# Performance work log

Hardware: AMD Instinct MI355X
Metric: run time of the kernel (lower is better)

## Reference

```python
import jax, jax.numpy as jnp
import numpy as np

N, M = 100000, 12
A, E = 128, 64
BN_EPS = 1e-5

def batchnorm(x, gamma, beta):
    # training-mode BN over leading dim, biased variance (torch default)
    mean = jnp.mean(x, axis=0)
    var = jnp.var(x, axis=0)
    return (x - mean) * jax.lax.rsqrt(var + BN_EPS) * gamma + beta

def setup_inputs() -> dict:
    key = jax.random.key(0)
    ks = jax.random.split(key, 9)
    s_in = 1.0 / np.sqrt(2 * A + E)
    s_skip = 1.0 / np.sqrt(A)
    return {
        "atom_in_fea": jax.random.normal(ks[0], (N, A), jnp.float32),
        "nbr_fea": jax.random.normal(ks[1], (N, M, E), jnp.float32),
        "nbr_fea_idx": jax.random.randint(ks[2], (N, M), 0, N),
        "W_full": jax.random.uniform(ks[3], (2 * A + E, 2 * A), jnp.float32, -s_in, s_in),
        "b_full": jax.random.uniform(ks[4], (2 * A,), jnp.float32, -s_in, s_in),
        "gamma1": jnp.ones((2 * A,), jnp.float32),
        "beta1": jnp.zeros((2 * A,), jnp.float32),
        "gamma2": jnp.ones((A,), jnp.float32),
        "beta2": jnp.zeros((A,), jnp.float32),
        "W_skip": jax.random.uniform(ks[5], (A, A), jnp.float32, -s_skip, s_skip),
        "b_skip": jax.random.uniform(ks[6], (A,), jnp.float32, -s_skip, s_skip),
    }

def reference(atom_in_fea, nbr_fea, nbr_fea_idx, W_full, b_full,
              gamma1, beta1, gamma2, beta2, W_skip, b_skip):
    atom_nbr_fea = atom_in_fea[nbr_fea_idx]                      # [N,M,A] gather
    atom_self_fea = jnp.broadcast_to(atom_in_fea[:, None, :], (N, M, A))
    total = jnp.concatenate([atom_self_fea, atom_nbr_fea, nbr_fea], axis=2)  # [N,M,2A+E]
    gated = jnp.einsum('nmf,fg->nmg', total, W_full) + b_full    # [N,M,2A]
    gated = batchnorm(gated.reshape(-1, 2 * A), gamma1, beta1).reshape(N, M, 2 * A)
    nbr_filter, nbr_core = gated[..., :A], gated[..., A:]
    nbr_sumed = jnp.sum(jax.nn.sigmoid(nbr_filter) * jax.nn.softplus(nbr_core), axis=1)  # [N,A]
    nbr_sumed = batchnorm(nbr_sumed, gamma2, beta2)
    skip_val = atom_in_fea @ W_skip + b_skip
    return jax.nn.softplus(skip_val + nbr_sumed)
```

## Files before the change

### kernel.cpp

```cpp
#include <hip/hip_runtime.h>
#include <stdint.h>

#define N_ATOM 100000
#define M_NBR 12
#define A_FEA 128
#define E_FEA 64
#define KDIM 320
#define GDIM 256
#define ROWS (N_ATOM*M_NBR)
#define BN_EPS 1e-5f

typedef unsigned short u16;
typedef unsigned int u32;
typedef __attribute__((ext_vector_type(8))) short short8;
typedef __attribute__((ext_vector_type(4))) float f32x4;

#define S_BN1SUM 0
#define S_BN1SSQ 256
#define S_S1 512
#define S_T1 768
#define S_BN2SUM 1024
#define S_BN2SSQ 1152
#define S_S2 1280
#define S_T2 1408
#define STATS_F32 1536

#define WPQ_OFF 0
#define W3_OFF 131072
#define WSK_OFF 163840
#define STATS_OFF 196608
#define P_OFF 202752
#define PQ_BYTES ((size_t)N_ATOM*256*2)
#define Q_OFF (P_OFF + PQ_BYTES)
#define NEED_MID (Q_OFF + PQ_BYTES)

__device__ __forceinline__ u16 f2bf(float x) {
    union { float f; u32 u; } v; v.f = x;
    u32 r = v.u + 0x7FFFu + ((v.u >> 16) & 1u);
    return (u16)(r >> 16);
}
__device__ __forceinline__ float bf2f(u16 u) {
    union { u32 u; float f; } v; v.u = ((u32)u) << 16;
    return v.f;
}
__device__ __forceinline__ float softplus_f(float x) {
    return fmaxf(x, 0.f) + __logf(1.f + __expf(-fabsf(x)));
}
__device__ __forceinline__ float sigmoid_f(float x) {
    return 1.f / (1.f + __expf(-x));
}

__global__ void zero_stats(float* __restrict__ stats) {
    int t = threadIdx.x;
    stats[t] = 0.f;
    stats[256 + t] = 0.f;
    stats[1024 + t] = 0.f;
}

__global__ void finalize1(const float* __restrict__ g1, const float* __restrict__ b1,
                          float* __restrict__ stats) {
    int c = threadIdx.x;
    const float inv_cnt = 1.f / (float)ROWS;
    float mean = stats[S_BN1SUM + c] * inv_cnt;
    float var  = stats[S_BN1SSQ + c] * inv_cnt - mean * mean;
    float iv = rsqrtf(var + BN_EPS);
    float s = g1[c] * iv;
    stats[S_S1 + c] = s;
    stats[S_T1 + c] = fmaf(-mean, s, b1[c]);
}

__global__ void finalize2(const float* __restrict__ g2, const float* __restrict__ b2,
                          float* __restrict__ stats) {
    int c = threadIdx.x;
    const float inv_cnt = 1.f / (float)N_ATOM;
    float mean = stats[S_BN2SUM + c] * inv_cnt;
    float var  = stats[S_BN2SSQ + c] * inv_cnt - mean * mean;
    float iv = rsqrtf(var + BN_EPS);
    float s = g2[c] * iv;
    stats[S_S2 + c] = s;
    stats[S_T2 + c] = fmaf(-mean, s, b2[c]);
}

__global__ void prep_pack_fast(const float* __restrict__ Wfull,
                               const float* __restrict__ Wskip,
                               u16* __restrict__ wpq, u16* __restrict__ w3,
                               u16* __restrict__ wsk) {
    int tid = blockIdx.x * blockDim.x + threadIdx.x;
    int l = tid & 63, fr = l & 15, fq = l >> 4;
    if (tid < 8192) {
        int ct = (tid >> 6) & 31;
        int kt = tid >> 11;
        int c = ct * 16 + fr;
        int k0 = kt * 32 + fq * 8;
        u16 tmp[8];
        #pragma unroll
        for (int i = 0; i < 8; ++i) {
            int kk = k0 + i;
            float v = (c < 256) ? Wfull[kk * GDIM + c]
                                : Wfull[(128 + kk) * GDIM + (c - 256)];
            tmp[i] = f2bf(v);
        }
        uint4 pk;
        pk.x = (u32)tmp[0] | ((u32)tmp[1] << 16);
        pk.y = (u32)tmp[2] | ((u32)tmp[3] << 16);
        pk.z = (u32)tmp[4] | ((u32)tmp[5] << 16);
        pk.w = (u32)tmp[6] | ((u32)tmp[7] << 16);
        *reinterpret_cast<uint4*>(&wpq[tid * 8]) = pk;
    } else if (tid < 10240) {
        int t2 = tid - 8192;
        int ct = (t2 >> 6) & 15;
        int kt = t2 >> 10;
        int c = ct * 16 + fr;
        int k0 = kt * 32 + fq * 8;
        u16 tmp[8];
        #pragma unroll
        for (int i = 0; i < 8; ++i) tmp[i] = f2bf(Wfull[(256 + k0 + i) * GDIM + c]);
        uint4 pk;
        pk.x = (u32)tmp[0] | ((u32)tmp[1] << 16);
        pk.y = (u32)tmp[2] | ((u32)tmp[3] << 16);
        pk.z = (u32)tmp[4] | ((u32)tmp[5] << 16);
        pk.w = (u32)tmp[6] | ((u32)tmp[7] << 16);
        *reinterpret_cast<uint4*>(&w3[t2 * 8]) = pk;
    } else if (tid < 12288) {
        int t3 = tid - 10240;
        int ct = (t3 >> 6) & 7;
        int kt = t3 >> 9;
        int c = ct * 16 + fr;
        int k0 = kt * 32 + fq * 8;
        u16 tmp[8];
        #pragma unroll
        for (int i = 0; i < 8; ++i) tmp[i] = f2bf(Wskip[(k0 + i) * A_FEA + c]);
        uint4 pk;
        pk.x = (u32)tmp[0] | ((u32)tmp[1] << 16);
        pk.y = (u32)tmp[2] | ((u32)tmp[3] << 16);
        pk.z = (u32)tmp[4] | ((u32)tmp[5] << 16);
        pk.w = (u32)tmp[6] | ((u32)tmp[7] << 16);
        *reinterpret_cast<uint4*>(&wsk[t3 * 8]) = pk;
    }
}

__launch_bounds__(256)
__global__ void pq_kernel(const float* __restrict__ atom_in,
                          const u16* __restrict__ wpq,
                          u16* __restrict__ Pb, u16* __restrict__ Qb) {
    __shared__ u16 al[64 * 130];
    const int t = threadIdx.x;
    const int w = t >> 6, l = t & 63, fr = l & 15, fq = l >> 4;
    const int n0 = blockIdx.x * 64;

    #pragma unroll
    for (int it = 0; it < 4; ++it) {
        int c = t + it * 256;
        int row = c >> 4, seg = c & 15;
        int n = n0 + row;
        uint4 pk = {0u, 0u, 0u, 0u};
        if (n < N_ATOM) {
            const float* src = atom_in + (size_t)n * A_FEA + seg * 8;
            float4 x0 = *reinterpret_cast<const float4*>(src);
            float4 x1 = *reinterpret_cast<const float4*>(src + 4);
            pk.x = (u32)f2bf(x0.x) | ((u32)f2bf(x0.y) << 16);
            pk.y = (u32)f2bf(x0.z) | ((u32)f2bf(x0.w) << 16);
            pk.z = (u32)f2bf(x1.x) | ((u32)f2bf(x1.y) << 16);
            pk.w = (u32)f2bf(x1.z) | ((u32)f2bf(x1.w) << 16);
        }
        *reinterpret_cast<uint4*>(&al[row * 130 + seg * 8]) = pk;
    }
    __syncthreads();

    f32x4 acc[4][8];
    #pragma unroll
    for (int rt = 0; rt < 4; ++rt)
        #pragma unroll
        for (int p = 0; p < 8; ++p)
            acc[rt][p] = (f32x4){0.f,0.f,0.f,0.f};

    for (int kt = 0; kt < 4; ++kt) {
        short8 af[4], bf[8];
        #pragma unroll
        for (int rt = 0; rt < 4; ++rt)
            af[rt] = *reinterpret_cast<const short8*>(
                &al[(rt * 16 + fr) * 130 + kt * 32 + fq * 8]);
        #pragma unroll
        for (int p = 0; p < 8; ++p)
            bf[p] = *reinterpret_cast<const short8*>(
                &wpq[((kt * 32 + w * 8 + p) * 64 + l) * 8]);
        #pragma unroll
        for (int rt = 0; rt < 4; ++rt)
            #pragma unroll
            for (int p = 0; p < 8; ++p)
                acc[rt][p] = __builtin_amdgcn_mfma_f32_16x16x32_bf16(
                    af[rt], bf[p], acc[rt][p], 0, 0, 0);
    }

    #pragma unroll
    for (int p = 0; p < 8; ++p) {
        int col = w * 128 + p * 16 + fr;
        u16* dst = (col < 256) ? Pb : Qb;
        int cc = (col < 256) ? col : (col - 256);
        #pragma unroll
        for (int rt = 0; rt < 4; ++rt)
            #pragma unroll
            for (int j = 0; j < 4; ++j) {
                int n = n0 + rt * 16 + fq * 4 + j;
                if (n < N_ATOM) dst[(size_t)n * 256 + cc] = f2bf(acc[rt][p][j]);
            }
    }
}

#define NTILES_E (ROWS/96)
#define GRID_E 2500
#define EPAD 66
#define PPAD 264
#define QPAD 268
#define ACTPAD2 134
#define P_SH (96*EPAD*2)
#define Q_SH (P_SH + 8*PPAD*2)
#define SH_TOTAL (Q_SH + 96*QPAD*2)

template<int MODE>
__launch_bounds__(512, 4)
__global__ void estage2(const float* __restrict__ nbr_fea,
                        const int* __restrict__ nbr_idx,
                        const u16* __restrict__ w3,
                        const u16* __restrict__ Pb,
                        const u16* __restrict__ Qb,
                        float* __restrict__ stats,
                        float* __restrict__ out_ns) {
    __shared__ __align__(16) unsigned char shraw[SH_TOTAL];
    u16* e_lds = (u16*)shraw;
    u16* p_lds = (u16*)(shraw + P_SH);
    u16* q_lds = (u16*)(shraw + Q_SH);
    float* act = (float*)(shraw + Q_SH);
    float* red = (float*)shraw;

    const int t = threadIdx.x;
    const int w = t >> 6, l = t & 63, fr = l & 15, fq = l >> 4;
    const int col0 = w * 16 + fr;
    const int col1 = 128 + col0;

    float s1v0 = 0.f, t1v0 = 0.f, s1v1 = 0.f, t1v1 = 0.f;
    if (MODE == 2) {
        s1v0 = stats[S_S1 + col0]; t1v0 = stats[S_T1 + col0];
        s1v1 = stats[S_S1 + col1]; t1v1 = stats[S_T1 + col1];
    }
    float ls0 = 0.f, lq0 = 0.f, ls1 = 0.f, lq1 = 0.f;
    float bsum = 0.f, bssq = 0.f;

    for (int tile = blockIdx.x; tile < NTILES_E; tile += GRID_E) {
        const int r0 = tile * 96;
        const int n0a = tile * 8;

        __syncthreads();

        #pragma unroll
        for (int i = 0; i < 2; ++i) {
            int o = t + i * 512;
            if (o < 768) {
                int row = o >> 3, seg = o & 7;
                const float* src = nbr_fea + (size_t)(r0 + row) * E_FEA + seg * 8;
                float4 x0 = *reinterpret_cast<const float4*>(src);
                float4 x1 = *reinterpret_cast<const float4*>(src + 4);
                uint4 pk;
                pk.x = (u32)f2bf(x0.x) | ((u32)f2bf(x0.y) << 16);
                pk.y = (u32)f2bf(x0.z) | ((u32)f2bf(x0.w) << 16);
                pk.z = (u32)f2bf(x1.x) | ((u32)f2bf(x1.y) << 16);
                pk.w = (u32)f2bf(x1.z) | ((u32)f2bf(x1.w) << 16);
                *reinterpret_cast<uint4*>(&e_lds[row * EPAD + seg * 8]) = pk;
            }
        }
        if (t < 256) {
            int row = t >> 5, seg = t & 31;
            *reinterpret_cast<uint4*>(&p_lds[row * PPAD + seg * 8]) =
                *reinterpret_cast<const uint4*>(&Pb[(size_t)(n0a + row) * 256 + seg * 8]);
        }
        #pragma unroll
        for (int i = 0; i < 12; ++i) {
            int row = i * 8 + w;
            int jr = nbr_idx[r0 + row];
            *reinterpret_cast<uint2*>(&q_lds[row * QPAD + l * 4]) =
                *reinterpret_cast<const uint2*>(&Qb[(size_t)jr * 256 + l * 4]);
        }
        __syncthreads();

        f32x4 acc[6][2];
        #pragma unroll
        for (int rt = 0; rt < 6; ++rt) {
            acc[rt][0] = (f32x4){0.f,0.f,0.f,0.f};
            acc[rt][1] = (f32x4){0.f,0.f,0.f,0.f};
        }
        #pragma unroll
        for (int kt = 0; kt < 2; ++kt) {
            short8 af[6], bf0, bf1;
            #pragma unroll
            for (int rt = 0; rt < 6; ++rt)
                af[rt] = *reinterpret_cast<const short8*>(
                    &e_lds[(rt * 16 + fr) * EPAD + kt * 32 + fq * 8]);
            bf0 = *reinterpret_cast<const short8*>(&w3[((kt * 16 + w) * 64 + l) * 8]);
            bf1 = *reinterpret_cast<const short8*>(&w3[((kt * 16 + 8 + w) * 64 + l) * 8]);
            #pragma unroll
            for (int rt = 0; rt < 6; ++rt) {
                acc[rt][0] = __builtin_amdgcn_mfma_f32_16x16x32_bf16(af[rt], bf0, acc[rt][0], 0, 0, 0);
                acc[rt][1] = __builtin_amdgcn_mfma_f32_16x16x32_bf16(af[rt], bf1, acc[rt][1], 0, 0, 0);
            }
        }

        if (MODE == 1) {
            #pragma unroll
            for (int rt = 0; rt < 6; ++rt)
                #pragma unroll
                for (int j = 0; j < 4; ++j) {
                    int row = rt * 16 + fq * 4 + j;
                    int atom = (row * 171) >> 11;
                    float g0 = acc[rt][0][j] + bf2f(p_lds[atom * PPAD + col0])
                                             + bf2f(q_lds[row * QPAD + col0]);
                    float g1 = acc[rt][1][j] + bf2f(p_lds[atom * PPAD + col1])
                                             + bf2f(q_lds[row * QPAD + col1]);
                    ls0 += g0; lq0 = fmaf(g0, g0, lq0);
                    ls1 += g1; lq1 = fmaf(g1, g1, lq1);
                }
        } else {
            float ar[24];
            #pragma unroll
            for (int rt = 0; rt < 6; ++rt)
                #pragma unroll
                for (int j = 0; j < 4; ++j) {
                    int row = rt * 16 + fq * 4 + j;
                    int atom = (row * 171) >> 11;
                    float g0 = acc[rt][0][j] + bf2f(p_lds[atom * PPAD + col0])
                                             + bf2f(q_lds[row * QPAD + col0]);
                    float g1 = acc[rt][1][j] + bf2f(p_lds[atom * PPAD + col1])
                                             + bf2f(q_lds[row * QPAD + col1]);
                    float gf = fmaf(g0, s1v0, t1v0);
                    float gc = fmaf(g1, s1v1, t1v1);
                    ar[rt * 4 + j] = sigmoid_f(gf) * softplus_f(gc);
                }
            __syncthreads();
            #pragma unroll
            for (int rt = 0; rt < 6; ++rt)
                #pragma unroll
                for (int j = 0; j < 4; ++j) {
                    int row = rt * 16 + fq * 4 + j;
                    act[row * ACTPAD2 + col0] = ar[rt * 4 + j];
                }
            __syncthreads();
            #pragma unroll
            for (int i = 0; i < 2; ++i) {
                int o = i * 512 + t;
                int a = o >> 7;
                int c = t & 127;
                float S = 0.f;
                #pragma unroll
                for (int mm = 0; mm < 12; ++mm)
                    S += act[(a * 12 + mm) * ACTPAD2 + c];
                out_ns[(size_t)(n0a + a) * A_FEA + c] = S;
                bsum += S;
                bssq = fmaf(S, S, bssq);
            }
        }
    }

    if (MODE == 1) {
        float s, q;
        s = ls0 + __shfl_xor(ls0, 16, 64); s += __shfl_xor(s, 32, 64);
        q = lq0 + __shfl_xor(lq0, 16, 64); q += __shfl_xor(q, 32, 64);
        if (fq == 0) {
            atomicAdd(&stats[S_BN1SUM + col0], s);
            atomicAdd(&stats[S_BN1SSQ + col0], q);
        }
        s = ls1 + __shfl_xor(ls1, 16, 64); s += __shfl_xor(s, 32, 64);
        q = lq1 + __shfl_xor(lq1, 16, 64); q += __shfl_xor(q, 32, 64);
        if (fq == 0) {
            atomicAdd(&stats[S_BN1SUM + col1], s);
            atomicAdd(&stats[S_BN1SSQ + col1], q);
        }
    } else {
        __syncthreads();
        if (t >= 128) {
            red[(t - 128) * 2]     = bsum;
            red[(t - 128) * 2 + 1] = bssq;
        }
        __syncthreads();
        if (t < 128) {
            bsum += red[t * 2]     + red[(128 + t) * 2]     + red[(256 + t) * 2];
            bssq += red[t * 2 + 1] + red[(128 + t) * 2 + 1] + red[(256 + t) * 2 + 1];
            atomicAdd(&stats[S_BN2SUM + t], bsum);
            atomicAdd(&stats[S_BN2SSQ + t], bssq);
        }
    }
}

#define BM5 64
__launch_bounds__(256, 2)
__global__ void skip_kernel(const float* __restrict__ atom_in,
                            const u16* __restrict__ wsf,
                            const float* __restrict__ b_skip,
                            const float* __restrict__ stats,
                            float* __restrict__ out) {
    __shared__ u16 a5[BM5 * 136];
    const int t = threadIdx.x;
    const int w = t >> 6, l = t & 63, fr = l & 15, fq = l >> 4;
    const int n0 = blockIdx.x * BM5;

    #pragma unroll
    for (int it = 0; it < 4; ++it) {
        int c = t + it * 256;
        int row = c >> 4, seg = c & 15;
        int n = n0 + row;
        uint4 pk = {0u, 0u, 0u, 0u};
        if (n < N_ATOM) {
            const float* src = atom_in + (size_t)n * A_FEA + seg * 8;
            float4 x0 = *reinterpret_cast<const float4*>(src);
            float4 x1 = *reinterpret_cast<const float4*>(src + 4);
            pk.x = (u32)f2bf(x0.x) | ((u32)f2bf(x0.y) << 16);
            pk.y = (u32)f2bf(x0.z) | ((u32)f2bf(x0.w) << 16);
            pk.z = (u32)f2bf(x1.x) | ((u32)f2bf(x1.y) << 16);
            pk.w = (u32)f2bf(x1.z) | ((u32)f2bf(x1.w) << 16);
        }
        *reinterpret_cast<uint4*>(&a5[row * 136 + seg * 8]) = pk;
    }
    __syncthreads();

    f32x4 acc[4][2];
    #pragma unroll
    for (int rt = 0; rt < 4; ++rt) {
        acc[rt][0] = (f32x4){0.f,0.f,0.f,0.f};
        acc[rt][1] = (f32x4){0.f,0.f,0.f,0.f};
    }
    for (int kt = 0; kt < 4; ++kt) {
        short8 af[4], bf[2];
        #pragma unroll
        for (int rt = 0; rt < 4; ++rt)
            af[rt] = *reinterpret_cast<const short8*>(
                &a5[(rt * 16 + fr) * 136 + kt * 32 + fq * 8]);
        #pragma unroll
        for (int p = 0; p < 2; ++p)
            bf[p] = *reinterpret_cast<const short8*>(
                &wsf[((kt * 8 + 2 * w + p) * 64 + l) * 8]);
        #pragma unroll
        for (int rt = 0; rt < 4; ++rt)
            #pragma unroll
            for (int p = 0; p < 2; ++p)
                acc[rt][p] = __builtin_amdgcn_mfma_f32_16x16x32_bf16(
                    af[rt], bf[p], acc[rt][p], 0, 0, 0);
    }

    #pragma unroll
    for (int p = 0; p < 2; ++p) {
        int col = w * 32 + p * 16 + fr;
        float bs = b_skip[col];
        float s2 = stats[S_S2 + col];
        float t2 = stats[S_T2 + col];
        #pragma unroll
        for (int rt = 0; rt < 4; ++rt)
            #pragma unroll
            for (int j = 0; j < 4; ++j) {
                int n = n0 + rt * 16 + fq * 4 + j;
                if (n < N_ATOM) {
                    size_t o = (size_t)n * A_FEA + col;
                    float S = out[o];
                    out[o] = softplus_f(acc[rt][p][j] + bs + fmaf(S, s2, t2));
                }
            }
    }
}

#define BM 96
#define NTILES (ROWS/BM)
#define GRID_P 2500
#define TPB 256
#define APAD 328
#define ACTPAD 132

__global__ void prep_pack_slow(const float* __restrict__ Wfull,
                               const float* __restrict__ Wskip,
                               u16* __restrict__ wf, u16* __restrict__ wsf) {
    int tid = blockIdx.x * blockDim.x + threadIdx.x;
    if (tid < 10240) {
        int l = tid & 63;
        int ct = (tid >> 6) & 15;
        int kt = tid >> 10;
        int fr = l & 15, fq = l >> 4;
        int col = ct * 16 + fr;
        int k0 = kt * 32 + fq * 8;
        u16 tmp[8];
        #pragma unroll
        for (int i = 0; i < 8; ++i) tmp[i] = f2bf(Wfull[(k0 + i) * GDIM + col]);
        uint4 pk;
        pk.x = (u32)tmp[0] | ((u32)tmp[1] << 16);
        pk.y = (u32)tmp[2] | ((u32)tmp[3] << 16);
        pk.z = (u32)tmp[4] | ((u32)tmp[5] << 16);
        pk.w = (u32)tmp[6] | ((u32)tmp[7] << 16);
        *reinterpret_cast<uint4*>(&wf[tid * 8]) = pk;
    } else if (tid < 12288) {
        int t2 = tid - 10240;
        int l = t2 & 63;
        int ct = (t2 >> 6) & 7;
        int kt = t2 >> 9;
        int fr = l & 15, fq = l >> 4;
        int col = ct * 16 + fr;
        int k0 = kt * 32 + fq * 8;
        u16 tmp[8];
        #pragma unroll
        for (int i = 0; i < 8; ++i) tmp[i] = f2bf(Wskip[(k0 + i) * A_FEA + col]);
        uint4 pk;
        pk.x = (u32)tmp[0] | ((u32)tmp[1] << 16);
        pk.y = (u32)tmp[2] | ((u32)tmp[3] << 16);
        pk.z = (u32)tmp[4] | ((u32)tmp[5] << 16);
        pk.w = (u32)tmp[6] | ((u32)tmp[7] << 16);
        *reinterpret_cast<uint4*>(&wsf[t2 * 8]) = pk;
    }
}

template<int PASS>
__launch_bounds__(TPB, 2)
__global__ void pass_kernel(const float* __restrict__ atom_in,
                            const float* __restrict__ nbr_fea,
                            const int* __restrict__ nbr_idx,
                            const u16* __restrict__ wf,
                            float* __restrict__ stats,
                            float* __restrict__ out_ns) {
    __shared__ union {
        u16 a[BM * APAD];
        float act[BM * ACTPAD];
    } sh;

    const int t = threadIdx.x;
    const int w = t >> 6, l = t & 63, fr = l & 15, fq = l >> 4;
    const int ct0 = 2 * w;

    int colp[4];
    colp[0] = ct0 * 16 + fr;
    colp[1] = colp[0] + 16;
    colp[2] = colp[0] + 128;
    colp[3] = colp[1] + 128;

    float s1v[4], t1v[4];
    if (PASS == 2) {
        #pragma unroll
        for (int p = 0; p < 4; ++p) {
            s1v[p] = stats[S_S1 + colp[p]];
            t1v[p] = stats[S_T1 + colp[p]];
        }
    }
    float ls[4] = {0.f,0.f,0.f,0.f}, lq[4] = {0.f,0.f,0.f,0.f};
    float bsum = 0.f, bssq = 0.f;

    for (int tile = blockIdx.x; tile < NTILES; tile += GRID_P) {
        const int n0 = tile * 8;

        __syncthreads();
        for (int it = 0; it < 15; ++it) {
            int c = t + it * TPB;
            int row = c / 40;
            int seg = c - row * 40;
            int an = row / 12;
            int m  = row - an * 12;
            int na = n0 + an;
            const float* src;
            if (seg < 16) {
                src = atom_in + (size_t)na * A_FEA + seg * 8;
            } else if (seg < 32) {
                int j = nbr_idx[na * M_NBR + m];
                src = atom_in + (size_t)j * A_FEA + (seg - 16) * 8;
            } else {
                src = nbr_fea + ((size_t)na * M_NBR + m) * E_FEA + (seg - 32) * 8;
            }
            float4 x0 = *reinterpret_cast<const float4*>(src);
            float4 x1 = *reinterpret_cast<const float4*>(src + 4);
            uint4 pk;
            pk.x = (u32)f2bf(x0.x) | ((u32)f2bf(x0.y) << 16);
            pk.y = (u32)f2bf(x0.z) | ((u32)f2bf(x0.w) << 16);
            pk.z = (u32)f2bf(x1.x) | ((u32)f2bf(x1.y) << 16);
            pk.w = (u32)f2bf(x1.z) | ((u32)f2bf(x1.w) << 16);
            *reinterpret_cast<uint4*>(&sh.a[row * APAD + seg * 8]) = pk;
        }
        __syncthreads();

        f32x4 acc[6][4];
        #pragma unroll
        for (int rt = 0; rt < 6; ++rt)
            #pragma unroll
            for (int p = 0; p < 4; ++p)
                acc[rt][p] = (f32x4){0.f,0.f,0.f,0.f};

        for (int kt = 0; kt < 10; ++kt) {
            short8 af[6], bf[4];
            #pragma unroll
            for (int rt = 0; rt < 6; ++rt)
                af[rt] = *reinterpret_cast<const short8*>(
                    &sh.a[(rt * 16 + fr) * APAD + kt * 32 + fq * 8]);
            #pragma unroll
            for (int p = 0; p < 4; ++p) {
                int ct = (p < 2) ? (ct0 + p) : (ct0 + 8 + (p - 2));
                bf[p] = *reinterpret_cast<const short8*>(
                    &wf[((kt * 16 + ct) * 64 + l) * 8]);
            }
            #pragma unroll
            for (int rt = 0; rt < 6; ++rt)
                #pragma unroll
                for (int p = 0; p < 4; ++p)
                    acc[rt][p] = __builtin_amdgcn_mfma_f32_16x16x32_bf16(
                        af[rt], bf[p], acc[rt][p], 0, 0, 0);
        }

        if (PASS == 1) {
            #pragma unroll
            for (int p = 0; p < 4; ++p)
                #pragma unroll
                for (int rt = 0; rt < 6; ++rt)
                    #pragma unroll
                    for (int j = 0; j < 4; ++j) {
                        float v = acc[rt][p][j];
                        ls[p] += v;
                        lq[p] = fmaf(v, v, lq[p]);
                    }
        } else {
            __syncthreads();
            #pragma unroll
            for (int rt = 0; rt < 6; ++rt)
                #pragma unroll
                for (int p = 0; p < 2; ++p)
                    #pragma unroll
                    for (int j = 0; j < 4; ++j) {
                        float gf = fmaf(acc[rt][p][j],     s1v[p],     t1v[p]);
                        float gc = fmaf(acc[rt][2 + p][j], s1v[2 + p], t1v[2 + p]);
                        float a = sigmoid_f(gf) * softplus_f(gc);
                        int row = rt * 16 + fq * 4 + j;
                        int colact = ct0 * 16 + p * 16 + fr;
                        sh.act[row * ACTPAD + colact] = a;
                    }
            __syncthreads();
            #pragma unroll
            for (int i = 0; i < 4; ++i) {
                int o = i * TPB + t;
                int a = o >> 7;
                int c = o & 127;
                float S = 0.f;
                #pragma unroll
                for (int mm = 0; mm < 12; ++mm)
                    S += sh.act[(a * 12 + mm) * ACTPAD + c];
                out_ns[(size_t)(n0 + a) * A_FEA + c] = S;
                bsum += S;
                bssq = fmaf(S, S, bssq);
            }
        }
    }

    if (PASS == 1) {
        #pragma unroll
        for (int p = 0; p < 4; ++p) {
            float s = ls[p], q = lq[p];
            s += __shfl_xor(s, 16, 64);
            s += __shfl_xor(s, 32, 64);
            q += __shfl_xor(q, 16, 64);
            q += __shfl_xor(q, 32, 64);
            if (fq == 0) {
                atomicAdd(&stats[S_BN1SUM + colp[p]], s);
                atomicAdd(&stats[S_BN1SSQ + colp[p]], q);
            }
        }
    } else {
        __syncthreads();
        if (t >= 128) {
            sh.act[(t - 128) * 2]     = bsum;
            sh.act[(t - 128) * 2 + 1] = bssq;
        }
        __syncthreads();
        if (t < 128) {
            bsum += sh.act[t * 2];
            bssq += sh.act[t * 2 + 1];
            atomicAdd(&stats[S_BN2SUM + t], bsum);
            atomicAdd(&stats[S_BN2SSQ + t], bssq);
        }
    }
}

extern "C" void kernel_launch(void* const* d_in, const int* in_sizes, int n_in,
                              void* d_out, int out_size, void* d_ws, size_t ws_size,
                              hipStream_t stream) {
    (void)in_sizes; (void)n_in; (void)out_size;
    const float* atom_in = (const float*)d_in[0];
    const float* nbr_fea = (const float*)d_in[1];
    const int*   nbr_idx = (const int*)d_in[2];
    const float* Wfull   = (const float*)d_in[3];
    const float* g1      = (const float*)d_in[5];
    const float* b1      = (const float*)d_in[6];
    const float* g2      = (const float*)d_in[7];
    const float* b2      = (const float*)d_in[8];
    const float* Wsk     = (const float*)d_in[9];
    const float* bsk     = (const float*)d_in[10];
    float* out = (float*)d_out;

    float* stats = (float*)((char*)d_ws + STATS_OFF);
    u16* wskf = (u16*)((char*)d_ws + WSK_OFF);

    if (ws_size >= NEED_MID) {
        u16* wpq = (u16*)d_ws;
        u16* w3  = (u16*)((char*)d_ws + W3_OFF);
        u16* Pb  = (u16*)((char*)d_ws + P_OFF);
        u16* Qb  = (u16*)((char*)d_ws + Q_OFF);

        zero_stats<<<1, 256, 0, stream>>>(stats);
        prep_pack_fast<<<48, 256, 0, stream>>>(Wfull, Wsk, wpq, w3, wskf);
        pq_kernel<<<(N_ATOM + 63) / 64, 256, 0, stream>>>(atom_in, wpq, Pb, Qb);
        estage2<1><<<GRID_E, 512, 0, stream>>>(nbr_fea, nbr_idx, w3, Pb, Qb, stats, out);
        finalize1<<<1, 256, 0, stream>>>(g1, b1, stats);
        estage2<2><<<GRID_E, 512, 0, stream>>>(nbr_fea, nbr_idx, w3, Pb, Qb, stats, out);
        finalize2<<<1, 128, 0, stream>>>(g2, b2, stats);
        skip_kernel<<<(N_ATOM + BM5 - 1) / BM5, 256, 0, stream>>>(atom_in, wskf, bsk, stats, out);
    } else {
        u16* wf = (u16*)d_ws;
        zero_stats<<<1, 256, 0, stream>>>(stats);
        prep_pack_slow<<<48, 256, 0, stream>>>(Wfull, Wsk, wf, wskf);
        pass_kernel<1><<<GRID_P, TPB, 0, stream>>>(atom_in, nbr_fea, nbr_idx, wf, stats, out);
        finalize1<<<1, 256, 0, stream>>>(g1, b1, stats);
        pass_kernel<2><<<GRID_P, TPB, 0, stream>>>(atom_in, nbr_fea, nbr_idx, wf, stats, out);
        finalize2<<<1, 128, 0, stream>>>(g2, b2, stats);
        skip_kernel<<<(N_ATOM + BM5 - 1) / BM5, 256, 0, stream>>>(atom_in, wskf, bsk, stats, out);
    }
}
```

Measured before the change: 853.6 us.

## Pre-convert neighbor features to bf16 once and transpose edge-stage MFMA operands

Measured after the change: 1.216 ms. 42.5% more time.

```diff
diff --git a/kernel.cpp b/kernel.cpp
--- a/kernel.cpp
+++ b/kernel.cpp
@@ -14,6 +14,7 @@
 typedef unsigned int u32;
 typedef __attribute__((ext_vector_type(8))) short short8;
 typedef __attribute__((ext_vector_type(4))) float f32x4;
+typedef __attribute__((ext_vector_type(4))) unsigned int u32x4;
 
 #define S_BN1SUM 0
 #define S_BN1SSQ 256
@@ -26,23 +27,30 @@
 #define STATS_F32 1536
 
 #define WPQ_OFF 0
-#define W3_OFF 131072
+#define W3T_OFF 131072
 #define WSK_OFF 163840
 #define STATS_OFF 196608
 #define P_OFF 202752
 #define PQ_BYTES ((size_t)N_ATOM*256*2)
 #define Q_OFF (P_OFF + PQ_BYTES)
-#define NEED_MID (Q_OFF + PQ_BYTES)
+#define NBF_OFF (P_OFF + 2*PQ_BYTES)
+#define NBF_BYTES ((size_t)ROWS*E_FEA*2)
+#define NEED_FAST2 (NBF_OFF + NBF_BYTES)
 
 __device__ __forceinline__ u16 f2bf(float x) {
     union { float f; u32 u; } v; v.f = x;
     u32 r = v.u + 0x7FFFu + ((v.u >> 16) & 1u);
     return (u16)(r >> 16);
 }
+__device__ __forceinline__ u16 f2bf_u(u32 u) {
+    return (u16)((u + 0x7FFFu + ((u >> 16) & 1u)) >> 16);
+}
 __device__ __forceinline__ float bf2f(u16 u) {
     union { u32 u; float f; } v; v.u = ((u32)u) << 16;
     return v.f;
 }
+__device__ __forceinline__ float bflo(u32 x) { return __uint_as_float(x << 16); }
+__device__ __forceinline__ float bfhi(u32 x) { return __uint_as_float(x & 0xFFFF0000u); }
 __device__ __forceinline__ float softplus_f(float x) {
     return fmaxf(x, 0.f) + __logf(1.f + __expf(-fabsf(x)));
 }
@@ -81,10 +89,25 @@
     stats[S_T2 + c] = fmaf(-mean, s, b2[c]);
 }
 
-__global__ void prep_pack_fast(const float* __restrict__ Wfull,
-                               const float* __restrict__ Wskip,
-                               u16* __restrict__ wpq, u16* __restrict__ w3,
-                               u16* __restrict__ wsk) {
+#define NBF_CHUNKS (ROWS*E_FEA/8)
+__global__ void conv_nbf(const float* __restrict__ nf, u16* __restrict__ nbf) {
+    size_t i = (size_t)blockIdx.x * blockDim.x + threadIdx.x;
+    if (i >= NBF_CHUNKS) return;
+    const u32x4* src = reinterpret_cast<const u32x4*>(nf + i * 8);
+    u32x4 a = __builtin_nontemporal_load(src);
+    u32x4 b = __builtin_nontemporal_load(src + 1);
+    u32x4 pk;
+    pk.x = (u32)f2bf_u(a.x) | ((u32)f2bf_u(a.y) << 16);
+    pk.y = (u32)f2bf_u(a.z) | ((u32)f2bf_u(a.w) << 16);
+    pk.z = (u32)f2bf_u(b.x) | ((u32)f2bf_u(b.y) << 16);
+    pk.w = (u32)f2bf_u(b.z) | ((u32)f2bf_u(b.w) << 16);
+    *reinterpret_cast<u32x4*>(&nbf[i * 8]) = pk;
+}
+
+__global__ void prep_pack2(const float* __restrict__ Wfull,
+                           const float* __restrict__ Wskip,
+                           u16* __restrict__ wpq, u16* __restrict__ w3t,
+                           u16* __restrict__ wsk) {
     int tid = blockIdx.x * blockDim.x + threadIdx.x;
     int l = tid & 63, fr = l & 15, fq = l >> 4;
     if (tid < 8192) {
@@ -108,19 +131,19 @@
         *reinterpret_cast<uint4*>(&wpq[tid * 8]) = pk;
     } else if (tid < 10240) {
         int t2 = tid - 8192;
-        int ct = (t2 >> 6) & 15;
-        int kt = t2 >> 10;
-        int c = ct * 16 + fr;
+        int frag = t2 >> 6;
+        int rt16 = frag & 15, kt = frag >> 4;
+        int gcol = rt16 * 16 + fr;
         int k0 = kt * 32 + fq * 8;
         u16 tmp[8];
         #pragma unroll
-        for (int i = 0; i < 8; ++i) tmp[i] = f2bf(Wfull[(256 + k0 + i) * GDIM + c]);
+        for (int i = 0; i < 8; ++i) tmp[i] = f2bf(Wfull[(256 + k0 + i) * GDIM + gcol]);
         uint4 pk;
         pk.x = (u32)tmp[0] | ((u32)tmp[1] << 16);
         pk.y = (u32)tmp[2] | ((u32)tmp[3] << 16);
         pk.z = (u32)tmp[4] | ((u32)tmp[5] << 16);
         pk.w = (u32)tmp[6] | ((u32)tmp[7] << 16);
-        *reinterpret_cast<uint4*>(&w3[t2 * 8]) = pk;
+        *reinterpret_cast<uint4*>(&w3t[t2 * 8]) = pk;
     } else if (tid < 12288) {
         int t3 = tid - 10240;
         int ct = (t3 >> 6) & 7;
@@ -210,40 +233,54 @@
 #define NTILES_E (ROWS/96)
 #define GRID_E 2500
 #define EPAD 66
-#define PPAD 264
-#define QPAD 268
-#define ACTPAD2 134
-#define P_SH (96*EPAD*2)
-#define Q_SH (P_SH + 8*PPAD*2)
-#define SH_TOTAL (Q_SH + 96*QPAD*2)
+#define PPAD2 264
+#define QPAD2 268
+#define ACT2 132
+#define E_SH (96*EPAD*2)
+#define P_SH0 E_SH
+#define Q_SH0 (E_SH + 8*PPAD2*2)
+#define SH_TOT (Q_SH0 + 96*QPAD2*2)
 
 template<int MODE>
 __launch_bounds__(512, 4)
-__global__ void estage2(const float* __restrict__ nbr_fea,
+__global__ void estage3(const u16* __restrict__ nbf,
                         const int* __restrict__ nbr_idx,
-                        const u16* __restrict__ w3,
+                        const u16* __restrict__ w3t,
                         const u16* __restrict__ Pb,
                         const u16* __restrict__ Qb,
                         float* __restrict__ stats,
                         float* __restrict__ out_ns) {
-    __shared__ __align__(16) unsigned char shraw[SH_TOTAL];
+    __shared__ __align__(16) unsigned char shraw[SH_TOT];
     u16* e_lds = (u16*)shraw;
-    u16* p_lds = (u16*)(shraw + P_SH);
-    u16* q_lds = (u16*)(shraw + Q_SH);
-    float* act = (float*)(shraw + Q_SH);
+    u16* p_lds = (u16*)(shraw + P_SH0);
+    u16* q_lds = (u16*)(shraw + Q_SH0);
+    float* act = (float*)(shraw + Q_SH0);
     float* red = (float*)shraw;
 
     const int t = threadIdx.x;
     const int w = t >> 6, l = t & 63, fr = l & 15, fq = l >> 4;
-    const int col0 = w * 16 + fr;
-    const int col1 = 128 + col0;
-
-    float s1v0 = 0.f, t1v0 = 0.f, s1v1 = 0.f, t1v1 = 0.f;
+    const int gbase0 = w * 16 + fq * 4;
+
+    short8 aw[2][2];
+    #pragma unroll
+    for (int kt = 0; kt < 2; ++kt)
+        #pragma unroll
+        for (int rt = 0; rt < 2; ++rt)
+            aw[kt][rt] = *reinterpret_cast<const short8*>(
+                &w3t[(((kt * 16) + w + rt * 8) * 64 + l) * 8]);
+
+    float s1v[2][4], t1v[2][4];
     if (MODE == 2) {
-        s1v0 = stats[S_S1 + col0]; t1v0 = stats[S_T1 + col0];
-        s1v1 = stats[S_S1 + col1]; t1v1 = stats[S_T1 + col1];
-    }
-    float ls0 = 0.f, lq0 = 0.f, ls1 = 0.f, lq1 = 0.f;
+        #pragma unroll
+        for (int rt = 0; rt < 2; ++rt)
+            #pragma unroll
+            for (int j = 0; j < 4; ++j) {
+                int col = gbase0 + rt * 128 + j;
+                s1v[rt][j] = stats[S_S1 + col];
+                t1v[rt][j] = stats[S_T1 + col];
+            }
+    }
+    float ls[2][4] = {{0,0,0,0},{0,0,0,0}}, lq[2][4] = {{0,0,0,0},{0,0,0,0}};
     float bsum = 0.f, bssq = 0.f;
 
     for (int tile = blockIdx.x; tile < NTILES_E; tile += GRID_E) {
@@ -257,91 +294,96 @@
             int o = t + i * 512;
             if (o < 768) {
                 int row = o >> 3, seg = o & 7;
-                const float* src = nbr_fea + (size_t)(r0 + row) * E_FEA + seg * 8;
-                float4 x0 = *reinterpret_cast<const float4*>(src);
-                float4 x1 = *reinterpret_cast<const float4*>(src + 4);
-                uint4 pk;
-                pk.x = (u32)f2bf(x0.x) | ((u32)f2bf(x0.y) << 16);
-                pk.y = (u32)f2bf(x0.z) | ((u32)f2bf(x0.w) << 16);
-                pk.z = (u32)f2bf(x1.x) | ((u32)f2bf(x1.y) << 16);
-                pk.w = (u32)f2bf(x1.z) | ((u32)f2bf(x1.w) << 16);
-                *reinterpret_cast<uint4*>(&e_lds[row * EPAD + seg * 8]) = pk;
+                uint4 v = *reinterpret_cast<const uint4*>(
+                    &nbf[(size_t)(r0 + row) * E_FEA + seg * 8]);
+                *reinterpret_cast<uint4*>(&e_lds[row * EPAD + seg * 8]) = v;
             }
         }
         if (t < 256) {
             int row = t >> 5, seg = t & 31;
-            *reinterpret_cast<uint4*>(&p_lds[row * PPAD + seg * 8]) =
+            *reinterpret_cast<uint4*>(&p_lds[row * PPAD2 + seg * 8]) =
                 *reinterpret_cast<const uint4*>(&Pb[(size_t)(n0a + row) * 256 + seg * 8]);
         }
         #pragma unroll
         for (int i = 0; i < 12; ++i) {
             int row = i * 8 + w;
             int jr = nbr_idx[r0 + row];
-            *reinterpret_cast<uint2*>(&q_lds[row * QPAD + l * 4]) =
+            *reinterpret_cast<uint2*>(&q_lds[row * QPAD2 + l * 4]) =
                 *reinterpret_cast<const uint2*>(&Qb[(size_t)jr * 256 + l * 4]);
         }
         __syncthreads();
 
-        f32x4 acc[6][2];
-        #pragma unroll
-        for (int rt = 0; rt < 6; ++rt) {
-            acc[rt][0] = (f32x4){0.f,0.f,0.f,0.f};
-            acc[rt][1] = (f32x4){0.f,0.f,0.f,0.f};
-        }
+        f32x4 acc[2][6];
+        #pragma unroll
+        for (int rt = 0; rt < 2; ++rt)
+            #pragma unroll
+            for (int ct = 0; ct < 6; ++ct)
+                acc[rt][ct] = (f32x4){0.f,0.f,0.f,0.f};
         #pragma unroll
         for (int kt = 0; kt < 2; ++kt) {
-            short8 af[6], bf0, bf1;
-            #pragma unroll
-            for (int rt = 0; rt < 6; ++rt)
-                af[rt] = *reinterpret_cast<const short8*>(
-                    &e_lds[(rt * 16 + fr) * EPAD + kt * 32 + fq * 8]);
-            bf0 = *reinterpret_cast<const short8*>(&w3[((kt * 16 + w) * 64 + l) * 8]);
-            bf1 = *reinterpret_cast<const short8*>(&w3[((kt * 16 + 8 + w) * 64 + l) * 8]);
-            #pragma unroll
-            for (int rt = 0; rt < 6; ++rt) {
-                acc[rt][0] = __builtin_amdgcn_mfma_f32_16x16x32_bf16(af[rt], bf0, acc[rt][0], 0, 0, 0);
-                acc[rt][1] = __builtin_amdgcn_mfma_f32_16x16x32_bf16(af[rt], bf1, acc[rt][1], 0, 0, 0);
-            }
+            short8 bf[6];
+            #pragma unroll
+            for (int ct = 0; ct < 6; ++ct)
+                bf[ct] = *reinterpret_cast<const short8*>(
+                    &e_lds[(ct * 16 + fr) * EPAD + kt * 32 + fq * 8]);
+            #pragma unroll
+            for (int rt = 0; rt < 2; ++rt)
+                #pragma unroll
+                for (int ct = 0; ct < 6; ++ct)
+                    acc[rt][ct] = __builtin_amdgcn_mfma_f32_16x16x32_bf16(
+                        aw[kt][rt], bf[ct], acc[rt][ct], 0, 0, 0);
         }
 
         if (MODE == 1) {
             #pragma unroll
-            for (int rt = 0; rt < 6; ++rt)
-                #pragma unroll
-                for (int j = 0; j < 4; ++j) {
-                    int row = rt * 16 + fq * 4 + j;
-                    int atom = (row * 171) >> 11;
-                    float g0 = acc[rt][0][j] + bf2f(p_lds[atom * PPAD + col0])
-                                             + bf2f(q_lds[row * QPAD + col0]);
-                    float g1 = acc[rt][1][j] + bf2f(p_lds[atom * PPAD + col1])
-                                             + bf2f(q_lds[row * QPAD + col1]);
-                    ls0 += g0; lq0 = fmaf(g0, g0, lq0);
-                    ls1 += g1; lq1 = fmaf(g1, g1, lq1);
-                }
+            for (int ct = 0; ct < 6; ++ct) {
+                int edge = ct * 16 + fr;
+                int atom = (edge * 171) >> 11;
+                uint2 qv0 = *reinterpret_cast<const uint2*>(&q_lds[edge * QPAD2 + gbase0]);
+                uint2 qv1 = *reinterpret_cast<const uint2*>(&q_lds[edge * QPAD2 + gbase0 + 128]);
+                uint2 pv0 = *reinterpret_cast<const uint2*>(&p_lds[atom * PPAD2 + gbase0]);
+                uint2 pv1 = *reinterpret_cast<const uint2*>(&p_lds[atom * PPAD2 + gbase0 + 128]);
+                float g;
+                g = acc[0][ct][0] + bflo(qv0.x) + bflo(pv0.x); ls[0][0] += g; lq[0][0] = fmaf(g,g,lq[0][0]);
+                g = acc[0][ct][1] + bfhi(qv0.x) + bfhi(pv0.x); ls[0][1] += g; lq[0][1] = fmaf(g,g,lq[0][1]);
+                g = acc[0][ct][2] + bflo(qv0.y) + bflo(pv0.y); ls[0][2] += g; lq[0][2] = fmaf(g,g,lq[0][2]);
+                g = acc[0][ct][3] + bfhi(qv0.y) + bfhi(pv0.y); ls[0][3] += g; lq[0][3] = fmaf(g,g,lq[0][3]);
+                g = acc[1][ct][0] + bflo(qv1.x) + bflo(pv1.x); ls[1][0] += g; lq[1][0] = fmaf(g,g,lq[1][0]);
+                g = acc[1][ct][1] + bfhi(qv1.x) + bfhi(pv1.x); ls[1][1] += g; lq[1][1] = fmaf(g,g,lq[1][1]);
+                g = acc[1][ct][2] + bflo(qv1.y) + bflo(pv1.y); ls[1][2] += g; lq[1][2] = fmaf(g,g,lq[1][2]);
+                g = acc[1][ct][3] + bfhi(qv1.y) + bfhi(pv1.y); ls[1][3] += g; lq[1][3] = fmaf(g,g,lq[1][3]);
+            }
         } else {
-            float ar[24];
-            #pragma unroll
-            for (int rt = 0; rt < 6; ++rt)
-                #pragma unroll
-                for (int j = 0; j < 4; ++j) {
-                    int row = rt * 16 + fq * 4 + j;
-                    int atom = (row * 171) >> 11;
-                    float g0 = acc[rt][0][j] + bf2f(p_lds[atom * PPAD + col0])
-                                             + bf2f(q_lds[row * QPAD + col0]);
-                    float g1 = acc[rt][1][j] + bf2f(p_lds[atom * PPAD + col1])
-                                             + bf2f(q_lds[row * QPAD + col1]);
-                    float gf = fmaf(g0, s1v0, t1v0);
-                    float gc = fmaf(g1, s1v1, t1v1);
-                    ar[rt * 4 + j] = sigmoid_f(gf) * softplus_f(gc);
-                }
+            float ar[6][4];
+            #pragma unroll
+            for (int ct = 0; ct < 6; ++ct) {
+                int edge = ct * 16 + fr;
+                int atom = (edge * 171) >> 11;
+                uint2 qv0 = *reinterpret_cast<const uint2*>(&q_lds[edge * QPAD2 + gbase0]);
+                uint2 qv1 = *reinterpret_cast<const uint2*>(&q_lds[edge * QPAD2 + gbase0 + 128]);
+                uint2 pv0 = *reinterpret_cast<const uint2*>(&p_lds[atom * PPAD2 + gbase0]);
+                uint2 pv1 = *reinterpret_cast<const uint2*>(&p_lds[atom * PPAD2 + gbase0 + 128]);
+                float gf, gc;
+                gf = acc[0][ct][0] + bflo(qv0.x) + bflo(pv0.x);
+                gc = acc[1][ct][0] + bflo(qv1.x) + bflo(pv1.x);
+                ar[ct][0] = sigmoid_f(fmaf(gf, s1v[0][0], t1v[0][0])) * softplus_f(fmaf(gc, s1v[1][0], t1v[1][0]));
+                gf = acc[0][ct][1] + bfhi(qv0.x) + bfhi(pv0.x);
+                gc = acc[1][ct][1] + bfhi(qv1.x) + bfhi(pv1.x);
+                ar[ct][1] = sigmoid_f(fmaf(gf, s1v[0][1], t1v[0][1])) * softplus_f(fmaf(gc, s1v[1][1], t1v[1][1]));
+                gf = acc[0][ct][2] + bflo(qv0.y) + bflo(pv0.y);
+                gc = acc[1][ct][2] + bflo(qv1.y) + bflo(pv1.y);
+                ar[ct][2] = sigmoid_f(fmaf(gf, s1v[0][2], t1v[0][2])) * softplus_f(fmaf(gc, s1v[1][2], t1v[1][2]));
+                gf = acc[0][ct][3] + bfhi(qv0.y) + bfhi(pv0.y);
+                gc = acc[1][ct][3] + bfhi(qv1.y) + bfhi(pv1.y);
+                ar[ct][3] = sigmoid_f(fmaf(gf, s1v[0][3], t1v[0][3])) * softplus_f(fmaf(gc, s1v[1][3], t1v[1][3]));
+            }
             __syncthreads();
             #pragma unroll
-            for (int rt = 0; rt < 6; ++rt)
-                #pragma unroll
-                for (int j = 0; j < 4; ++j) {
-                    int row = rt * 16 + fq * 4 + j;
-                    act[row * ACTPAD2 + col0] = ar[rt * 4 + j];
-                }
+            for (int ct = 0; ct < 6; ++ct) {
+                int edge = ct * 16 + fr;
+                float4 f4 = make_float4(ar[ct][0], ar[ct][1], ar[ct][2], ar[ct][3]);
+                *reinterpret_cast<float4*>(&act[edge * ACT2 + gbase0]) = f4;
+            }
             __syncthreads();
             #pragma unroll
             for (int i = 0; i < 2; ++i) {
@@ -351,7 +393,7 @@
                 float S = 0.f;
                 #pragma unroll
                 for (int mm = 0; mm < 12; ++mm)
-                    S += act[(a * 12 + mm) * ACTPAD2 + c];
+                    S += act[(a * 12 + mm) * ACT2 + c];
                 out_ns[(size_t)(n0a + a) * A_FEA + c] = S;
                 bsum += S;
                 bssq = fmaf(S, S, bssq);
@@ -360,19 +402,21 @@
     }
 
     if (MODE == 1) {
-        float s, q;
-        s = ls0 + __shfl_xor(ls0, 16, 64); s += __shfl_xor(s, 32, 64);
-        q = lq0 + __shfl_xor(lq0, 16, 64); q += __shfl_xor(q, 32, 64);
-        if (fq == 0) {
-            atomicAdd(&stats[S_BN1SUM + col0], s);
-            atomicAdd(&stats[S_BN1SSQ + col0], q);
-        }
-        s = ls1 + __shfl_xor(ls1, 16, 64); s += __shfl_xor(s, 32, 64);
-        q = lq1 + __shfl_xor(lq1, 16, 64); q += __shfl_xor(q, 32, 64);
-        if (fq == 0) {
-            atomicAdd(&stats[S_BN1SUM + col1], s);
-            atomicAdd(&stats[S_BN1SSQ + col1], q);
-        }
+        #pragma unroll
+        for (int rt = 0; rt < 2; ++rt)
+            #pragma unroll
+            for (int j = 0; j < 4; ++j) {
+                float s = ls[rt][j], q = lq[rt][j];
+                s += __shfl_xor(s, 1, 64);  s += __shfl_xor(s, 2, 64);
+                s += __shfl_xor(s, 4, 64);  s += __shfl_xor(s, 8, 64);
+                q += __shfl_xor(q, 1, 64);  q += __shfl_xor(q, 2, 64);
+                q += __shfl_xor(q, 4, 64);  q += __shfl_xor(q, 8, 64);
+                if (fr == 0) {
+                    int col = gbase0 + rt * 128 + j;
+                    atomicAdd(&stats[S_BN1SUM + col], s);
+                    atomicAdd(&stats[S_BN1SSQ + col], q);
+                }
+            }
     } else {
         __syncthreads();
         if (t >= 128) {
@@ -694,18 +738,20 @@
     float* stats = (float*)((char*)d_ws + STATS_OFF);
     u16* wskf = (u16*)((char*)d_ws + WSK_OFF);
 
-    if (ws_size >= NEED_MID) {
+    if (ws_size >= NEED_FAST2) {
         u16* wpq = (u16*)d_ws;
-        u16* w3  = (u16*)((char*)d_ws + W3_OFF);
+        u16* w3t = (u16*)((char*)d_ws + W3T_OFF);
         u16* Pb  = (u16*)((char*)d_ws + P_OFF);
         u16* Qb  = (u16*)((char*)d_ws + Q_OFF);
+        u16* nbf = (u16*)((char*)d_ws + NBF_OFF);
 
         zero_stats<<<1, 256, 0, stream>>>(stats);
-        prep_pack_fast<<<48, 256, 0, stream>>>(Wfull, Wsk, wpq, w3, wskf);
+        prep_pack2<<<48, 256, 0, stream>>>(Wfull, Wsk, wpq, w3t, wskf);
         pq_kernel<<<(N_ATOM + 63) / 64, 256, 0, stream>>>(atom_in, wpq, Pb, Qb);
-        estage2<1><<<GRID_E, 512, 0, stream>>>(nbr_fea, nbr_idx, w3, Pb, Qb, stats, out);
+        conv_nbf<<<(NBF_CHUNKS + 255) / 256, 256, 0, stream>>>(nbr_fea, nbf);
+        estage3<1><<<GRID_E, 512, 0, stream>>>(nbf, nbr_idx, w3t, Pb, Qb, stats, out);
         finalize1<<<1, 256, 0, stream>>>(g1, b1, stats);
-        estage2<2><<<GRID_E, 512, 0, stream>>>(nbr_fea, nbr_idx, w3, Pb, Qb, stats, out);
+        estage3<2><<<GRID_E, 512, 0, stream>>>(nbf, nbr_idx, w3t, Pb, Qb, stats, out);
         finalize2<<<1, 128, 0, stream>>>(g2, b2, stats);
         skip_kernel<<<(N_ATOM + BM5 - 1) / BM5, 256, 0, stream>>>(atom_in, wskf, bsk, stats, out);
     } else {
```
